# Optimization experiments

Hardware: AMD Instinct MI355X
Metric: run time of the kernel (lower is better)

Reference implementation:

```python
import jax, jax.numpy as jnp
import numpy as np

B, N, L, S, D, H = 16, 8, 64, 32, 256, 128  # 2*H == D required by the module


def _lstm_dir(seq, Wih, Whh, bih, bhh):
    # seq: [T, B, D] -> hidden states [T, B, H]; PyTorch gate order i,f,g,o
    Hd = Whh.shape[1]
    b = seq.shape[1]

    def step(carry, xt):
        h, c = carry
        gates = xt @ Wih.T + h @ Whh.T + bih + bhh  # [B, 4H]
        i, f, g, o = jnp.split(gates, 4, axis=-1)
        c = jax.nn.sigmoid(f) * c + jax.nn.sigmoid(i) * jnp.tanh(g)
        h = jax.nn.sigmoid(o) * jnp.tanh(c)
        return (h, c), h

    init = (jnp.zeros((b, Hd), seq.dtype), jnp.zeros((b, Hd), seq.dtype))
    _, hs = jax.lax.scan(step, init, seq)
    return hs


def setup_inputs() -> dict:
    key = jax.random.key(0)
    ks = jax.random.split(key, 16)
    sc = 1.0 / np.sqrt(D)
    sch = 1.0 / np.sqrt(H)
    inp = {
        "x": jax.random.normal(ks[0], (B, N, L, D), jnp.float32),
        "s": jax.random.normal(ks[1], (B, S, D), jnp.float32),
        # co-attention params (Linear(dim,dim,bias=False) stored [out,in])
        "W": jax.random.normal(ks[2], (D, D), jnp.float32) * sc,
        "U": jax.random.normal(ks[3], (D, D), jnp.float32) * sc,
        "v": jax.random.normal(ks[4], (D,), jnp.float32) * sc,
        # BiLSTM params, forward and backward directions
        "Wih_f": jax.random.normal(ks[5], (4 * H, D), jnp.float32) * sch,
        "Whh_f": jax.random.normal(ks[6], (4 * H, H), jnp.float32) * sch,
        "bih_f": jax.random.normal(ks[7], (4 * H,), jnp.float32) * sch,
        "bhh_f": jax.random.normal(ks[8], (4 * H,), jnp.float32) * sch,
        "Wih_b": jax.random.normal(ks[9], (4 * H, D), jnp.float32) * sch,
        "Whh_b": jax.random.normal(ks[10], (4 * H, H), jnp.float32) * sch,
        "bih_b": jax.random.normal(ks[11], (4 * H,), jnp.float32) * sch,
        "bhh_b": jax.random.normal(ks[12], (4 * H,), jnp.float32) * sch,
        # self-attention params (Linear(D,D) with bias, Linear(D,1) no bias)
        "saW": jax.random.normal(ks[13], (D, D), jnp.float32) * sc,
        "sab": jax.random.normal(ks[14], (D,), jnp.float32) * sc,
        "sav": jax.random.normal(ks[15], (D,), jnp.float32) * sc,
    }
    return inp


def reference(x, s, W, U, v, Wih_f, Whh_f, bih_f, bhh_f,
              Wih_b, Whh_b, bih_b, bhh_b, saW, sab, sav):
    # ---- CoAttention (vectorized over B, N, S) ----
    Wx = jnp.einsum('bnld,ed->bnle', x, W)          # [B,N,L,D]
    Us = jnp.einsum('bsd,ed->bse', s, U)            # [B,S,D]
    # additive attention: tanh(Wx + Us) . v  -> scores over L
    e = jnp.tanh(Wx[:, :, None, :, :] + Us[:, None, :, None, :])  # [B,N,S,L,D]
    scores = jnp.einsum('bnsld,d->bnsl', e, v)      # [B,N,S,L]
    a = jax.nn.softmax(scores, axis=-1)             # softmax over L (dim=0 of [L,B] in torch)
    sr = jnp.einsum('bnsl,bnld->bnsd', a, x)        # [B,N,S,D]
    sr = sr.mean(axis=2)                            # [B,N,D]

    # ---- BiLSTM over the N axis ----
    u = jnp.swapaxes(sr, 0, 1)                      # [N,B,D]
    hf = _lstm_dir(u, Wih_f, Whh_f, bih_f, bhh_f)   # [N,B,H]
    hb = _lstm_dir(u[::-1], Wih_b, Whh_b, bih_b, bhh_b)[::-1]
    c = jnp.swapaxes(jnp.concatenate([hf, hb], axis=-1), 0, 1)  # [B,N,2H]

    # ---- Self-attention pooling ----
    att = jnp.tanh(c @ saW.T + sab) @ sav           # [B,N]
    att = jax.nn.softmax(att, axis=1)
    g = jnp.einsum('bn,bnd->bd', att, c)            # [B,2H]
    return g
```

## Files before the change

kernel.cpp:

```cpp
#include <hip/hip_runtime.h>
#include <cstddef>

#define Bsz 16
#define Nn  8
#define Ll  64
#define Ss  32
#define Dd  256
#define Hh  128

#define LOG2E 1.4426950408889634f

__device__ __forceinline__ float rcp_f(float x)  { return __builtin_amdgcn_rcpf(x); }
__device__ __forceinline__ float exp2_f(float x) { return __builtin_amdgcn_exp2f(x); }

__device__ __forceinline__ float fast_tanh(float x) {
    return 1.0f - 2.0f * rcp_f(exp2_f(x * (2.0f * LOG2E)) + 1.0f);
}
__device__ __forceinline__ float fast_sigmoid(float x) {
    return rcp_f(1.0f + exp2_f(-x * LOG2E));
}
__device__ __forceinline__ float wave_sum(float x) {
#pragma unroll
    for (int off = 32; off > 0; off >>= 1) x += __shfl_xor(x, off, 64);
    return x;
}
__device__ __forceinline__ float wave_max(float x) {
#pragma unroll
    for (int off = 32; off > 0; off >>= 1) x = fmaxf(x, __shfl_xor(x, off, 64));
    return x;
}

__device__ __forceinline__ void gemm_tile_128x64(const float* __restrict__ A,
                                                 const float* __restrict__ B,
                                                 float* __restrict__ C,
                                                 int ldc,
                                                 float (* __restrict__ As)[44],
                                                 float (* __restrict__ Bs)[44])
{
    const int tid = threadIdx.x;
    const int kq = tid & 7;
    const int mr = tid >> 3;
    const int tx = tid & 15;
    const int ty = tid >> 4;
    float acc[8][4] = {};
    for (int kc = 0; kc < 256; kc += 32) {
#pragma unroll
        for (int p = 0; p < 4; ++p) {
            float4 t = *(const float4*)&A[(size_t)(mr + 32 * p) * 256 + kc + kq * 4];
            *(float4*)&As[mr + 32 * p][kq * 4] = t;
        }
#pragma unroll
        for (int p = 0; p < 2; ++p) {
            float4 t = *(const float4*)&B[(size_t)(mr + 32 * p) * 256 + kc + kq * 4];
            *(float4*)&Bs[mr + 32 * p][kq * 4] = t;
        }
        __syncthreads();
#pragma unroll
        for (int kk = 0; kk < 32; kk += 4) {
            float4 br[4];
#pragma unroll
            for (int j = 0; j < 4; ++j) br[j] = *(const float4*)&Bs[tx + 16 * j][kk];
#pragma unroll
            for (int i = 0; i < 8; ++i) {
                float4 a = *(const float4*)&As[ty + 16 * i][kk];
#pragma unroll
                for (int j = 0; j < 4; ++j) {
                    acc[i][j] = fmaf(a.x, br[j].x, acc[i][j]);
                    acc[i][j] = fmaf(a.y, br[j].y, acc[i][j]);
                    acc[i][j] = fmaf(a.z, br[j].z, acc[i][j]);
                    acc[i][j] = fmaf(a.w, br[j].w, acc[i][j]);
                }
            }
        }
        __syncthreads();
    }
#pragma unroll
    for (int i = 0; i < 8; ++i)
#pragma unroll
        for (int j = 0; j < 4; ++j)
            C[(size_t)(ty + 16 * i) * ldc + tx + 16 * j] = acc[i][j];
}

__global__ __launch_bounds__(256) void gemm_stage1(const float* __restrict__ x,
                                                   const float* __restrict__ s,
                                                   const float* __restrict__ W,
                                                   const float* __restrict__ U,
                                                   float* __restrict__ Wx,
                                                   float* __restrict__ Us)
{
    __shared__ float As[128][44];
    __shared__ float Bs[64][44];
    int blk = blockIdx.x;
    const float *Ap, *Bp; float* Cp;
    if (blk < 256) {
        int my = blk >> 2, nx = blk & 3;
        Ap = x + (size_t)my * 128 * 256;
        Bp = W + (size_t)nx * 64 * 256;
        Cp = Wx + (size_t)my * 128 * 256 + nx * 64;
    } else {
        int b2 = blk - 256;
        int my = b2 >> 2, nx = b2 & 3;
        Ap = s + (size_t)my * 128 * 256;
        Bp = U + (size_t)nx * 64 * 256;
        Cp = Us + (size_t)my * 128 * 256 + nx * 64;
    }
    gemm_tile_128x64(Ap, Bp, Cp, 256, As, Bs);
}

__global__ __launch_bounds__(256) void gemm_gx(const float* __restrict__ sr,
                                               const float* __restrict__ Wf,
                                               const float* __restrict__ Wb,
                                               float* __restrict__ gx)
{
    __shared__ float As[128][44];
    __shared__ float Bs[64][44];
    int blk = blockIdx.x;
    int dir = blk >> 3, nx = blk & 7;
    const float* Bp = (dir ? Wb : Wf) + (size_t)nx * 64 * 256;
    gemm_tile_128x64(sr, Bp, gx + dir * 512 + nx * 64, 1024, As, Bs);
}

__global__ __launch_bounds__(512, 1) void scores_kernel(const float* __restrict__ Wx,
                                                        const float* __restrict__ Us,
                                                        const float* __restrict__ v,
                                                        float* __restrict__ a_buf)
{
    __shared__ float wx[64][260];
    __shared__ float us[16][256];
    __shared__ float sc[16][64];
    const int bid = blockIdx.x;
    const int bn = bid >> 1, sh = bid & 1;
    const int b = bn >> 3;
    const int tid = threadIdx.x;
    const int lane = tid & 63, w = tid >> 6;
    const float C2 = 2.0f * LOG2E;
    {
        const float* wxg = Wx + (size_t)bn * (Ll * Dd);
        int c = tid & 63, r0 = tid >> 6;
#pragma unroll
        for (int p = 0; p < 8; ++p) {
            int r = r0 + p * 8;
            float4 t = *(const float4*)&wxg[r * 256 + c * 4];
            t.x *= C2; t.y *= C2; t.z *= C2; t.w *= C2;
            *(float4*)&wx[r][c * 4] = t;
        }
        const float* usg = Us + ((size_t)b * Ss + sh * 16) * 256;
#pragma unroll
        for (int p = 0; p < 2; ++p) {
            int r = r0 + p * 8;
            float4 t = *(const float4*)&usg[r * 256 + c * 4];
            t.x *= C2; t.y *= C2; t.z *= C2; t.w *= C2;
            *(float4*)&us[r][c * 4] = t;
        }
    }
    __syncthreads();
    float4 v4 = *(const float4*)&v[lane * 4];
    float vsum = wave_sum(v4.x + v4.y + v4.z + v4.w);
    const int s0 = w * 2, s1 = s0 + 1;
    float4 ua = *(const float4*)&us[s0][lane * 4];
    float4 ub = *(const float4*)&us[s1][lane * 4];
    for (int l = 0; l < 64; ++l) {
        float4 wv = *(const float4*)&wx[l][lane * 4];
        float a0 =       v4.x * rcp_f(exp2_f(wv.x + ua.x) + 1.0f);
        a0 = fmaf(v4.y, rcp_f(exp2_f(wv.y + ua.y) + 1.0f), a0);
        a0 = fmaf(v4.z, rcp_f(exp2_f(wv.z + ua.z) + 1.0f), a0);
        a0 = fmaf(v4.w, rcp_f(exp2_f(wv.w + ua.w) + 1.0f), a0);
        float a1 =       v4.x * rcp_f(exp2_f(wv.x + ub.x) + 1.0f);
        a1 = fmaf(v4.y, rcp_f(exp2_f(wv.y + ub.y) + 1.0f), a1);
        a1 = fmaf(v4.z, rcp_f(exp2_f(wv.z + ub.z) + 1.0f), a1);
        a1 = fmaf(v4.w, rcp_f(exp2_f(wv.w + ub.w) + 1.0f), a1);
        a0 = wave_sum(a0);
        a1 = wave_sum(a1);
        if (lane == 0) { sc[s0][l] = vsum - 2.0f * a0; sc[s1][l] = vsum - 2.0f * a1; }
    }
    __syncthreads();
    float sv0 = sc[s0][lane], sv1 = sc[s1][lane];
    float e0 = exp2_f((sv0 - wave_max(sv0)) * LOG2E);
    float e1 = exp2_f((sv1 - wave_max(sv1)) * LOG2E);
    float i0 = rcp_f(wave_sum(e0));
    float i1 = rcp_f(wave_sum(e1));
    float* ab = a_buf + ((size_t)bn * Ss + sh * 16) * 64;
    ab[s0 * 64 + lane] = e0 * i0;
    ab[s1 * 64 + lane] = e1 * i1;
}

__global__ __launch_bounds__(256) void sr_kernel(const float* __restrict__ a_buf,
                                                 const float* __restrict__ x,
                                                 float* __restrict__ sr_nb)
{
    int bn = blockIdx.x;
    int b = bn >> 3, n = bn & 7;
    int tid = threadIdx.x;
    __shared__ float abar[64];
    __shared__ float red[4][64];
    {
        int l = tid & 63, sg = tid >> 6;
        float p = 0.f;
        for (int s = sg * 8; s < sg * 8 + 8; ++s)
            p += a_buf[((size_t)bn * 32 + s) * 64 + l];
        red[sg][l] = p;
        __syncthreads();
        if (tid < 64)
            abar[tid] = (red[0][tid] + red[1][tid] + red[2][tid] + red[3][tid]) * (1.0f / 32.0f);
        __syncthreads();
    }
    float acc = 0.f;
    const float* xp = x + (size_t)bn * Ll * Dd;
#pragma unroll 8
    for (int l = 0; l < Ll; ++l)
        acc = fmaf(abar[l], xp[l * Dd + tid], acc);
    sr_nb[((size_t)n * Bsz + b) * Dd + tid] = acc;
}

__global__ __launch_bounds__(512) void lstm_kernel(const float* __restrict__ gx,
                                                   const float* __restrict__ Whh_f,
                                                   const float* __restrict__ Whh_b,
                                                   const float* __restrict__ bih_f, const float* __restrict__ bhh_f,
                                                   const float* __restrict__ bih_b, const float* __restrict__ bhh_b,
                                                   float* __restrict__ h_out)
{
    int blk = blockIdx.x;
    int dir = blk >> 4, b = blk & 15;
    int g = threadIdx.x;
    const float* wr = ((dir == 0) ? Whh_f : Whh_b) + (size_t)g * 128;
    float4 w4[32];
#pragma unroll
    for (int k = 0; k < 32; ++k) w4[k] = ((const float4*)wr)[k];
    float bias = (dir == 0) ? (bih_f[g] + bhh_f[g]) : (bih_b[g] + bhh_b[g]);
    __shared__ float h[128], c[128], gb[512];
    if (g < 128) { h[g] = 0.f; c[g] = 0.f; }
    __syncthreads();
    for (int t = 0; t < Nn; ++t) {
        int n = (dir == 0) ? t : (Nn - 1 - t);
        float a0 = gx[((size_t)(n * Bsz + b)) * 1024 + dir * 512 + g] + bias;
        float a1 = 0.f, a2 = 0.f, a3 = 0.f;
#pragma unroll
        for (int k = 0; k < 32; ++k) {
            float4 hv = *(const float4*)&h[k * 4];
            a0 = fmaf(w4[k].x, hv.x, a0);
            a1 = fmaf(w4[k].y, hv.y, a1);
            a2 = fmaf(w4[k].z, hv.z, a2);
            a3 = fmaf(w4[k].w, hv.w, a3);
        }
        float pre = (a0 + a1) + (a2 + a3);
        float act = (g < 256 || g >= 384) ? fast_sigmoid(pre) : fast_tanh(pre);
        gb[g] = act;
        __syncthreads();
        if (g < 128) {
            float i_ = gb[g], f_ = gb[128 + g], g_ = gb[256 + g], o_ = gb[384 + g];
            float cn = fmaf(f_, c[g], i_ * g_);
            float hn = o_ * fast_tanh(cn);
            c[g] = cn; h[g] = hn;
            h_out[(((size_t)dir * Nn + n) * Bsz + b) * Hh + g] = hn;
        }
        __syncthreads();
    }
}

__global__ __launch_bounds__(256) void attpool_kernel(const float* __restrict__ hbuf,
                                                      const float* __restrict__ saW,
                                                      const float* __restrict__ sab,
                                                      const float* __restrict__ sav,
                                                      float* __restrict__ out)
{
    int b = blockIdx.x;
    int e = threadIdx.x;
    __shared__ float cvec[8][260];
    __shared__ float part[8][4];
#pragma unroll
    for (int n = 0; n < 8; ++n)
        cvec[n][e] = (e < 128) ? hbuf[((size_t)n * Bsz + b) * Hh + e]
                               : hbuf[((size_t)(Nn + n) * Bsz + b) * Hh + (e - 128)];
    __syncthreads();
    const float* wrow = saW + (size_t)e * 256;
    float acc[8];
    float b0 = sab[e];
#pragma unroll
    for (int n = 0; n < 8; ++n) acc[n] = b0;
#pragma unroll 2
    for (int dq0 = 0; dq0 < 8; ++dq0) {
        float4 wq[8];
#pragma unroll
        for (int q = 0; q < 8; ++q) wq[q] = *(const float4*)&wrow[dq0 * 32 + q * 4];
#pragma unroll
        for (int q = 0; q < 8; ++q) {
#pragma unroll
            for (int n = 0; n < 8; ++n) {
                float4 cv = *(const float4*)&cvec[n][dq0 * 32 + q * 4];
                acc[n] = fmaf(wq[q].x, cv.x, acc[n]);
                acc[n] = fmaf(wq[q].y, cv.y, acc[n]);
                acc[n] = fmaf(wq[q].z, cv.z, acc[n]);
                acc[n] = fmaf(wq[q].w, cv.w, acc[n]);
            }
        }
    }
    int w = e >> 6, lane = e & 63;
    float se = sav[e];
#pragma unroll
    for (int n = 0; n < 8; ++n) {
        float t = fast_tanh(acc[n]) * se;
        t = wave_sum(t);
        if (lane == 0) part[n][w] = t;
    }
    __syncthreads();
    float av[8], mx = -1e30f;
#pragma unroll
    for (int n = 0; n < 8; ++n) {
        av[n] = part[n][0] + part[n][1] + part[n][2] + part[n][3];
        mx = fmaxf(mx, av[n]);
    }
    float sum = 0.f;
#pragma unroll
    for (int n = 0; n < 8; ++n) { av[n] = exp2_f((av[n] - mx) * LOG2E); sum += av[n]; }
    float inv = rcp_f(sum);
    float acco = 0.f;
#pragma unroll
    for (int n = 0; n < 8; ++n) acco = fmaf(av[n], cvec[n][e], acco);
    out[b * 256 + e] = acco * inv;
}

extern "C" void kernel_launch(void* const* d_in, const int* in_sizes, int n_in,
                              void* d_out, int out_size, void* d_ws, size_t ws_size,
                              hipStream_t stream) {
    const float* x     = (const float*)d_in[0];
    const float* s     = (const float*)d_in[1];
    const float* W     = (const float*)d_in[2];
    const float* U     = (const float*)d_in[3];
    const float* v     = (const float*)d_in[4];
    const float* Wih_f = (const float*)d_in[5];
    const float* Whh_f = (const float*)d_in[6];
    const float* bih_f = (const float*)d_in[7];
    const float* bhh_f = (const float*)d_in[8];
    const float* Wih_b = (const float*)d_in[9];
    const float* Whh_b = (const float*)d_in[10];
    const float* bih_b = (const float*)d_in[11];
    const float* bhh_b = (const float*)d_in[12];
    const float* saW   = (const float*)d_in[13];
    const float* sab   = (const float*)d_in[14];
    const float* sav   = (const float*)d_in[15];
    float* out = (float*)d_out;
    float* ws  = (float*)d_ws;

    float* Wx    = ws;
    float* Us    = Wx + 2097152;
    float* a_buf = Us + 131072;
    float* sr_nb = a_buf + 262144;
    float* gx    = sr_nb + 32768;
    float* hbuf  = gx + 131072;

    hipLaunchKernelGGL(gemm_stage1, dim3(272), dim3(256), 0, stream, x, s, W, U, Wx, Us);
    hipLaunchKernelGGL(scores_kernel, dim3(256), dim3(512), 0, stream, Wx, Us, v, a_buf);
    hipLaunchKernelGGL(sr_kernel, dim3(128), dim3(256), 0, stream, a_buf, x, sr_nb);
    hipLaunchKernelGGL(gemm_gx, dim3(16), dim3(256), 0, stream, sr_nb, Wih_f, Wih_b, gx);
    hipLaunchKernelGGL(lstm_kernel, dim3(32), dim3(512), 0, stream,
                       gx, Whh_f, Whh_b, bih_f, bhh_f, bih_b, bhh_b, hbuf);
    hipLaunchKernelGGL(attpool_kernel, dim3(16), dim3(256), 0, stream, hbuf, saW, sab, sav, out);
}
```

Baseline: 213.2 us.

## Fuse scores with sr reduction and input projection into LSTM kernel

Merges the scores/softmax kernel with the weighted-sum sr kernel, so each block handles all 32 s rows for one (b,n) and the attention weights never go to global memory. The input-to-hidden projection moves into the LSTM kernel, removing the separate gx GEMM launch and its buffer. The 2*log2e prescale now happens in the stage-1 GEMM epilogue instead of when staging into LDS. In exchange the scores kernel runs with half as many blocks (128), and each LSTM thread does a serial 256-long dot product for 8 timesteps before the recurrence starts.

```diff
diff --git a/kernel.cpp b/kernel.cpp
--- a/kernel.cpp
+++ b/kernel.cpp
@@ -33,7 +33,7 @@
 __device__ __forceinline__ void gemm_tile_128x64(const float* __restrict__ A,
                                                  const float* __restrict__ B,
                                                  float* __restrict__ C,
-                                                 int ldc,
+                                                 int ldc, float oscale,
                                                  float (* __restrict__ As)[44],
                                                  float (* __restrict__ Bs)[44])
 {
@@ -78,7 +78,7 @@
     for (int i = 0; i < 8; ++i)
 #pragma unroll
         for (int j = 0; j < 4; ++j)
-            C[(size_t)(ty + 16 * i) * ldc + tx + 16 * j] = acc[i][j];
+            C[(size_t)(ty + 16 * i) * ldc + tx + 16 * j] = acc[i][j] * oscale;
 }
 
 __global__ __launch_bounds__(256) void gemm_stage1(const float* __restrict__ x,
@@ -104,135 +104,149 @@
         Bp = U + (size_t)nx * 64 * 256;
         Cp = Us + (size_t)my * 128 * 256 + nx * 64;
     }
-    gemm_tile_128x64(Ap, Bp, Cp, 256, As, Bs);
-}
-
-__global__ __launch_bounds__(256) void gemm_gx(const float* __restrict__ sr,
-                                               const float* __restrict__ Wf,
-                                               const float* __restrict__ Wb,
-                                               float* __restrict__ gx)
-{
-    __shared__ float As[128][44];
-    __shared__ float Bs[64][44];
-    int blk = blockIdx.x;
-    int dir = blk >> 3, nx = blk & 7;
-    const float* Bp = (dir ? Wb : Wf) + (size_t)nx * 64 * 256;
-    gemm_tile_128x64(sr, Bp, gx + dir * 512 + nx * 64, 1024, As, Bs);
-}
-
-__global__ __launch_bounds__(512, 1) void scores_kernel(const float* __restrict__ Wx,
-                                                        const float* __restrict__ Us,
-                                                        const float* __restrict__ v,
-                                                        float* __restrict__ a_buf)
+    gemm_tile_128x64(Ap, Bp, Cp, 256, 2.0f * LOG2E, As, Bs);
+}
+
+__global__ __launch_bounds__(512, 1) void scores_sr_kernel(const float* __restrict__ Wx,
+                                                           const float* __restrict__ Us,
+                                                           const float* __restrict__ v,
+                                                           const float* __restrict__ x,
+                                                           float* __restrict__ sr_out)
 {
     __shared__ float wx[64][260];
-    __shared__ float us[16][256];
-    __shared__ float sc[16][64];
-    const int bid = blockIdx.x;
-    const int bn = bid >> 1, sh = bid & 1;
-    const int b = bn >> 3;
+    __shared__ float us[32][256];
+    __shared__ float sc[32][64];
+    __shared__ float abar[64];
+    __shared__ float red[256];
+    const int bn = blockIdx.x;
+    const int b = bn >> 3, n = bn & 7;
     const int tid = threadIdx.x;
     const int lane = tid & 63, w = tid >> 6;
-    const float C2 = 2.0f * LOG2E;
     {
         const float* wxg = Wx + (size_t)bn * (Ll * Dd);
         int c = tid & 63, r0 = tid >> 6;
 #pragma unroll
         for (int p = 0; p < 8; ++p) {
             int r = r0 + p * 8;
-            float4 t = *(const float4*)&wxg[r * 256 + c * 4];
-            t.x *= C2; t.y *= C2; t.z *= C2; t.w *= C2;
-            *(float4*)&wx[r][c * 4] = t;
-        }
-        const float* usg = Us + ((size_t)b * Ss + sh * 16) * 256;
-#pragma unroll
-        for (int p = 0; p < 2; ++p) {
+            *(float4*)&wx[r][c * 4] = *(const float4*)&wxg[r * 256 + c * 4];
+        }
+        const float* usg = Us + (size_t)b * Ss * 256;
+#pragma unroll
+        for (int p = 0; p < 4; ++p) {
             int r = r0 + p * 8;
-            float4 t = *(const float4*)&usg[r * 256 + c * 4];
-            t.x *= C2; t.y *= C2; t.z *= C2; t.w *= C2;
-            *(float4*)&us[r][c * 4] = t;
+            *(float4*)&us[r][c * 4] = *(const float4*)&usg[r * 256 + c * 4];
         }
     }
     __syncthreads();
     float4 v4 = *(const float4*)&v[lane * 4];
     float vsum = wave_sum(v4.x + v4.y + v4.z + v4.w);
-    const int s0 = w * 2, s1 = s0 + 1;
-    float4 ua = *(const float4*)&us[s0][lane * 4];
-    float4 ub = *(const float4*)&us[s1][lane * 4];
+    const int s0 = w * 4;
+    float4 u0 = *(const float4*)&us[s0 + 0][lane * 4];
+    float4 u1 = *(const float4*)&us[s0 + 1][lane * 4];
+    float4 u2 = *(const float4*)&us[s0 + 2][lane * 4];
+    float4 u3 = *(const float4*)&us[s0 + 3][lane * 4];
     for (int l = 0; l < 64; ++l) {
         float4 wv = *(const float4*)&wx[l][lane * 4];
-        float a0 =       v4.x * rcp_f(exp2_f(wv.x + ua.x) + 1.0f);
-        a0 = fmaf(v4.y, rcp_f(exp2_f(wv.y + ua.y) + 1.0f), a0);
-        a0 = fmaf(v4.z, rcp_f(exp2_f(wv.z + ua.z) + 1.0f), a0);
-        a0 = fmaf(v4.w, rcp_f(exp2_f(wv.w + ua.w) + 1.0f), a0);
-        float a1 =       v4.x * rcp_f(exp2_f(wv.x + ub.x) + 1.0f);
-        a1 = fmaf(v4.y, rcp_f(exp2_f(wv.y + ub.y) + 1.0f), a1);
-        a1 = fmaf(v4.z, rcp_f(exp2_f(wv.z + ub.z) + 1.0f), a1);
-        a1 = fmaf(v4.w, rcp_f(exp2_f(wv.w + ub.w) + 1.0f), a1);
-        a0 = wave_sum(a0);
-        a1 = wave_sum(a1);
-        if (lane == 0) { sc[s0][l] = vsum - 2.0f * a0; sc[s1][l] = vsum - 2.0f * a1; }
-    }
-    __syncthreads();
-    float sv0 = sc[s0][lane], sv1 = sc[s1][lane];
-    float e0 = exp2_f((sv0 - wave_max(sv0)) * LOG2E);
-    float e1 = exp2_f((sv1 - wave_max(sv1)) * LOG2E);
-    float i0 = rcp_f(wave_sum(e0));
-    float i1 = rcp_f(wave_sum(e1));
-    float* ab = a_buf + ((size_t)bn * Ss + sh * 16) * 64;
-    ab[s0 * 64 + lane] = e0 * i0;
-    ab[s1 * 64 + lane] = e1 * i1;
-}
-
-__global__ __launch_bounds__(256) void sr_kernel(const float* __restrict__ a_buf,
-                                                 const float* __restrict__ x,
-                                                 float* __restrict__ sr_nb)
-{
-    int bn = blockIdx.x;
-    int b = bn >> 3, n = bn & 7;
-    int tid = threadIdx.x;
-    __shared__ float abar[64];
-    __shared__ float red[4][64];
+        float a0 =       v4.x * rcp_f(exp2_f(wv.x + u0.x) + 1.0f);
+        a0 = fmaf(v4.y, rcp_f(exp2_f(wv.y + u0.y) + 1.0f), a0);
+        a0 = fmaf(v4.z, rcp_f(exp2_f(wv.z + u0.z) + 1.0f), a0);
+        a0 = fmaf(v4.w, rcp_f(exp2_f(wv.w + u0.w) + 1.0f), a0);
+        float a1 =       v4.x * rcp_f(exp2_f(wv.x + u1.x) + 1.0f);
+        a1 = fmaf(v4.y, rcp_f(exp2_f(wv.y + u1.y) + 1.0f), a1);
+        a1 = fmaf(v4.z, rcp_f(exp2_f(wv.z + u1.z) + 1.0f), a1);
+        a1 = fmaf(v4.w, rcp_f(exp2_f(wv.w + u1.w) + 1.0f), a1);
+        float a2 =       v4.x * rcp_f(exp2_f(wv.x + u2.x) + 1.0f);
+        a2 = fmaf(v4.y, rcp_f(exp2_f(wv.y + u2.y) + 1.0f), a2);
+        a2 = fmaf(v4.z, rcp_f(exp2_f(wv.z + u2.z) + 1.0f), a2);
+        a2 = fmaf(v4.w, rcp_f(exp2_f(wv.w + u2.w) + 1.0f), a2);
+        float a3 =       v4.x * rcp_f(exp2_f(wv.x + u3.x) + 1.0f);
+        a3 = fmaf(v4.y, rcp_f(exp2_f(wv.y + u3.y) + 1.0f), a3);
+        a3 = fmaf(v4.z, rcp_f(exp2_f(wv.z + u3.z) + 1.0f), a3);
+        a3 = fmaf(v4.w, rcp_f(exp2_f(wv.w + u3.w) + 1.0f), a3);
+        a0 = wave_sum(a0); a1 = wave_sum(a1); a2 = wave_sum(a2); a3 = wave_sum(a3);
+        if (lane == 0) {
+            sc[s0 + 0][l] = vsum - 2.0f * a0;
+            sc[s0 + 1][l] = vsum - 2.0f * a1;
+            sc[s0 + 2][l] = vsum - 2.0f * a2;
+            sc[s0 + 3][l] = vsum - 2.0f * a3;
+        }
+    }
+    __syncthreads();
+#pragma unroll
+    for (int j = 0; j < 4; ++j) {
+        float sv = sc[s0 + j][lane];
+        float e = exp2_f((sv - wave_max(sv)) * LOG2E);
+        float inv = rcp_f(wave_sum(e));
+        sc[s0 + j][lane] = e * inv;
+    }
+    __syncthreads();
+    if (tid < 64) {
+        float acc = 0.f;
+#pragma unroll
+        for (int s = 0; s < 32; ++s) acc += sc[s][tid];
+        abar[tid] = acc * (1.0f / 32.0f);
+    }
+    __syncthreads();
     {
-        int l = tid & 63, sg = tid >> 6;
-        float p = 0.f;
-        for (int s = sg * 8; s < sg * 8 + 8; ++s)
-            p += a_buf[((size_t)bn * 32 + s) * 64 + l];
-        red[sg][l] = p;
-        __syncthreads();
-        if (tid < 64)
-            abar[tid] = (red[0][tid] + red[1][tid] + red[2][tid] + red[3][tid]) * (1.0f / 32.0f);
-        __syncthreads();
-    }
-    float acc = 0.f;
-    const float* xp = x + (size_t)bn * Ll * Dd;
+        int d = tid & 255, half = tid >> 8;
+        const float* xp = x + (size_t)bn * Ll * Dd;
+        float acc = 0.f;
 #pragma unroll 8
-    for (int l = 0; l < Ll; ++l)
-        acc = fmaf(abar[l], xp[l * Dd + tid], acc);
-    sr_nb[((size_t)n * Bsz + b) * Dd + tid] = acc;
-}
-
-__global__ __launch_bounds__(512) void lstm_kernel(const float* __restrict__ gx,
-                                                   const float* __restrict__ Whh_f,
-                                                   const float* __restrict__ Whh_b,
-                                                   const float* __restrict__ bih_f, const float* __restrict__ bhh_f,
-                                                   const float* __restrict__ bih_b, const float* __restrict__ bhh_b,
-                                                   float* __restrict__ h_out)
+        for (int l = half * 32; l < half * 32 + 32; ++l)
+            acc = fmaf(abar[l], xp[l * Dd + d], acc);
+        if (half == 1) red[d] = acc;
+        __syncthreads();
+        if (half == 0)
+            sr_out[((size_t)b * Nn + n) * Dd + d] = acc + red[d];
+    }
+}
+
+__global__ __launch_bounds__(512) void lstm_fused(const float* __restrict__ sr,
+                                                  const float* __restrict__ Wih_f,
+                                                  const float* __restrict__ Wih_b,
+                                                  const float* __restrict__ Whh_f,
+                                                  const float* __restrict__ Whh_b,
+                                                  const float* __restrict__ bih_f, const float* __restrict__ bhh_f,
+                                                  const float* __restrict__ bih_b, const float* __restrict__ bhh_b,
+                                                  float* __restrict__ h_out)
 {
     int blk = blockIdx.x;
     int dir = blk >> 4, b = blk & 15;
     int g = threadIdx.x;
+    __shared__ float s_lds[8][256];
+    __shared__ float h[128], c[128], gb[512];
+    {
+        int nr = g >> 6, off = (g & 63) * 4;
+        *(float4*)&s_lds[nr][off] = *(const float4*)&sr[((size_t)b * Nn + nr) * Dd + off];
+        if (g < 128) { h[g] = 0.f; c[g] = 0.f; }
+    }
+    __syncthreads();
+    const float* wih = ((dir == 0) ? Wih_f : Wih_b) + (size_t)g * 256;
+    const float* srow[8];
+#pragma unroll
+    for (int tt = 0; tt < 8; ++tt) srow[tt] = s_lds[dir ? 7 - tt : tt];
+    float gpre[8] = {};
+#pragma unroll
+    for (int kq = 0; kq < 64; ++kq) {
+        float4 wv = ((const float4*)wih)[kq];
+#pragma unroll
+        for (int tt = 0; tt < 8; ++tt) {
+            const float4 sv = *(const float4*)&srow[tt][kq * 4];
+            gpre[tt] = fmaf(wv.x, sv.x, gpre[tt]);
+            gpre[tt] = fmaf(wv.y, sv.y, gpre[tt]);
+            gpre[tt] = fmaf(wv.z, sv.z, gpre[tt]);
+            gpre[tt] = fmaf(wv.w, sv.w, gpre[tt]);
+        }
+    }
     const float* wr = ((dir == 0) ? Whh_f : Whh_b) + (size_t)g * 128;
     float4 w4[32];
 #pragma unroll
     for (int k = 0; k < 32; ++k) w4[k] = ((const float4*)wr)[k];
     float bias = (dir == 0) ? (bih_f[g] + bhh_f[g]) : (bih_b[g] + bhh_b[g]);
-    __shared__ float h[128], c[128], gb[512];
-    if (g < 128) { h[g] = 0.f; c[g] = 0.f; }
-    __syncthreads();
+    __syncthreads();
+#pragma unroll
     for (int t = 0; t < Nn; ++t) {
-        int n = (dir == 0) ? t : (Nn - 1 - t);
-        float a0 = gx[((size_t)(n * Bsz + b)) * 1024 + dir * 512 + g] + bias;
+        float a0 = gpre[t] + bias;
         float a1 = 0.f, a2 = 0.f, a3 = 0.f;
 #pragma unroll
         for (int k = 0; k < 32; ++k) {
@@ -251,6 +265,7 @@
             float cn = fmaf(f_, c[g], i_ * g_);
             float hn = o_ * fast_tanh(cn);
             c[g] = cn; h[g] = hn;
+            int n = dir ? (7 - t) : t;
             h_out[(((size_t)dir * Nn + n) * Bsz + b) * Hh + g] = hn;
         }
         __syncthreads();
@@ -343,16 +358,13 @@
 
     float* Wx    = ws;
     float* Us    = Wx + 2097152;
-    float* a_buf = Us + 131072;
-    float* sr_nb = a_buf + 262144;
-    float* gx    = sr_nb + 32768;
-    float* hbuf  = gx + 131072;
+    float* sr_nb = Us + 131072;
+    float* hbuf  = sr_nb + 32768;
 
     hipLaunchKernelGGL(gemm_stage1, dim3(272), dim3(256), 0, stream, x, s, W, U, Wx, Us);
-    hipLaunchKernelGGL(scores_kernel, dim3(256), dim3(512), 0, stream, Wx, Us, v, a_buf);
-    hipLaunchKernelGGL(sr_kernel, dim3(128), dim3(256), 0, stream, a_buf, x, sr_nb);
-    hipLaunchKernelGGL(gemm_gx, dim3(16), dim3(256), 0, stream, sr_nb, Wih_f, Wih_b, gx);
-    hipLaunchKernelGGL(lstm_kernel, dim3(32), dim3(512), 0, stream,
-                       gx, Whh_f, Whh_b, bih_f, bhh_f, bih_b, bhh_b, hbuf);
+    hipLaunchKernelGGL(scores_sr_kernel, dim3(128), dim3(512), 0, stream, Wx, Us, v, x, sr_nb);
+    hipLaunchKernelGGL(lstm_fused, dim3(32), dim3(512), 0, stream,
+                       sr_nb, Wih_f, Wih_b, Whh_f, Whh_b,
+                       bih_f, bhh_f, bih_b, bhh_b, hbuf);
     hipLaunchKernelGGL(attpool_kernel, dim3(16), dim3(256), 0, stream, hbuf, saW, sab, sav, out);
 }
```

Measured after the change: 224.2 us. 5.2% more time.
